# Kernel optimization log

Hardware: AMD Instinct MI355X
Metric: run time of the kernel (lower is better)

The kernel has to match this reference:

```python
import jax, jax.numpy as jnp
import numpy as np

N_IN, N_OUT, KNN, N_EL = 100000, 25000, 9, 200000
B, C_IN, C_OUT = 4, 8, 16


def setup_inputs() -> dict:
    key = jax.random.key(0)
    ks = jax.random.split(key, 16)
    M = N_OUT * KNN
    inp = {
        "features": jax.random.normal(ks[0], (B, C_IN, N_IN), jnp.float32),
        "domain_points": jax.random.uniform(ks[1], (N_IN, 2), jnp.float32),
        "range_points": jax.random.uniform(ks[2], (N_OUT, 2), jnp.float32),
        # kNN structure: each range point i has exactly KNN support edges
        "eval_idx_dst": jnp.repeat(jnp.arange(N_OUT, dtype=jnp.int32), KNN),
        "eval_idx_src": jax.random.randint(ks[3], (M,), 0, N_IN, jnp.int32),
        "element_list": jax.random.randint(ks[4], (N_EL, 3), 0, N_IN, jnp.int32),
        # Siren filter MLP: 2 -> 16 x5 -> C_IN*C_OUT (outermost linear)
        "siren_w_in": jax.random.normal(ks[5], (2, 16), jnp.float32) / jnp.sqrt(2.0),
        "siren_b_in": jax.random.normal(ks[6], (16,), jnp.float32) * 0.1,
        "siren_wh": jax.random.normal(ks[7], (4, 16, 16), jnp.float32) / 4.0,
        "siren_bh": jax.random.normal(ks[8], (4, 16), jnp.float32) * 0.1,
        "siren_w_out": jax.random.normal(ks[9], (16, C_IN * C_OUT), jnp.float32) / 4.0,
        "siren_b_out": jax.random.normal(ks[10], (C_IN * C_OUT,), jnp.float32) * 0.1,
        # weight_map: 6 -> 8 -> 8 -> 8 -> 3, all sigmoid
        "wm_w0": jax.random.normal(ks[11], (6, 8), jnp.float32) / jnp.sqrt(6.0),
        "wm_b0": jnp.zeros((8,), jnp.float32),
        "wm_w1": jax.random.normal(ks[12], (8, 8), jnp.float32) / jnp.sqrt(8.0),
        "wm_b1": jnp.zeros((8,), jnp.float32),
        "wm_w2": jax.random.normal(ks[13], (8, 8), jnp.float32) / jnp.sqrt(8.0),
        "wm_b2": jnp.zeros((8,), jnp.float32),
        "wm_w3": jax.random.normal(ks[14], (8, 3), jnp.float32) / jnp.sqrt(8.0),
        "wm_b3": jnp.zeros((3,), jnp.float32),
    }
    return inp


def reference(features, domain_points, range_points, eval_idx_src, eval_idx_dst,
              element_list, siren_w_in, siren_b_in, siren_wh, siren_bh,
              siren_w_out, siren_b_out, wm_w0, wm_b0, wm_w1, wm_b1,
              wm_w2, wm_b2, wm_w3, wm_b3):
    omega_0 = 1.0
    n_in = domain_points.shape[0]
    n_out = range_points.shape[0]
    c_in = features.shape[1]
    c_out = siren_w_out.shape[1] // c_in

    # --- eval_weight_map: per-element MLP + scatter_add to per-node weights ---
    el_pts = domain_points[element_list].reshape(element_list.shape[0], -1)  # [E, 6]
    h = jax.nn.sigmoid(el_pts @ wm_w0 + wm_b0)
    h = jax.nn.sigmoid(h @ wm_w1 + wm_b1)
    h = jax.nn.sigmoid(h @ wm_w2 + wm_b2)
    el_w = jax.nn.sigmoid(h @ wm_w3 + wm_b3)  # [E, 3]
    node_w = jax.ops.segment_sum(el_w.reshape(-1), element_list.reshape(-1),
                                 num_segments=n_in)  # [N_in]
    w = node_w[eval_idx_src]  # [M]

    # --- per-edge Siren filter on relative locations ---
    locs = range_points[eval_idx_dst] - domain_points[eval_idx_src]  # [M, 2]
    h = jnp.sin(omega_0 * (locs @ siren_w_in + siren_b_in))
    for i in range(siren_wh.shape[0]):  # fixed small layer count
        h = jnp.sin(omega_0 * (h @ siren_wh[i] + siren_bh[i]))
    filt = ((h @ siren_w_out + siren_b_out)
            .reshape(-1, c_in, c_out)) / c_in  # [M, C_in, C_out]

    # --- weighted gather -> contract -> scatter (quadrature integral) ---
    gathered = features[:, :, eval_idx_src]  # [B, C_in, M]
    values = jnp.einsum('n,nij,bin->bjn', w, filt, gathered)  # [B, C_out, M]
    seg = jax.ops.segment_sum(values.transpose(2, 0, 1), eval_idx_dst,
                              num_segments=n_out)  # [N_out, B, C_out]
    return seg.transpose(1, 2, 0)  # [B, C_out, N_out]
```

## Files before the change

kernel.cpp:

```cpp
#include <hip/hip_runtime.h>

#define N_IN   100000
#define N_OUT  25000
#define KNN    9
#define N_EL   200000
#define BB     4
#define C_IN   8
#define C_OUT  16

#define DPB  14
#define EPB  (DPB * KNN)
#define SOP  65
#define HST  17

__global__ void __launch_bounds__(256) elem_kernel(
    const int*   __restrict__ el,
    const float* __restrict__ dp,
    const float* __restrict__ w0, const float* __restrict__ b0,
    const float* __restrict__ w1, const float* __restrict__ b1,
    const float* __restrict__ w2, const float* __restrict__ b2,
    const float* __restrict__ w3, const float* __restrict__ b3,
    float* __restrict__ node_w)
{
    int e = blockIdx.x * 256 + threadIdx.x;
    if (e >= N_EL) return;
    int i0 = el[e*3+0], i1 = el[e*3+1], i2 = el[e*3+2];
    float2 p0 = ((const float2*)dp)[i0];
    float2 p1 = ((const float2*)dp)[i1];
    float2 p2 = ((const float2*)dp)[i2];
    float p[6] = { p0.x, p0.y, p1.x, p1.y, p2.x, p2.y };

    float h[8], h2[8];
#pragma unroll
    for (int k = 0; k < 8; ++k) {
        float t = b0[k];
#pragma unroll
        for (int j = 0; j < 6; ++j) t = fmaf(p[j], w0[j*8+k], t);
        h[k] = 1.f / (1.f + __expf(-t));
    }
#pragma unroll
    for (int k = 0; k < 8; ++k) {
        float t = b1[k];
#pragma unroll
        for (int j = 0; j < 8; ++j) t = fmaf(h[j], w1[j*8+k], t);
        h2[k] = 1.f / (1.f + __expf(-t));
    }
#pragma unroll
    for (int k = 0; k < 8; ++k) {
        float t = b2[k];
#pragma unroll
        for (int j = 0; j < 8; ++j) t = fmaf(h2[j], w2[j*8+k], t);
        h[k] = 1.f / (1.f + __expf(-t));
    }
    float o[3];
#pragma unroll
    for (int k = 0; k < 3; ++k) {
        float t = b3[k];
#pragma unroll
        for (int j = 0; j < 8; ++j) t = fmaf(h[j], w3[j*3+k], t);
        o[k] = 1.f / (1.f + __expf(-t));
    }
    atomicAdd(&node_w[i0], o[0]);
    atomicAdd(&node_w[i1], o[1]);
    atomicAdd(&node_w[i2], o[2]);
}

__global__ void __launch_bounds__(256) prep_kernel(
    const float* __restrict__ f, float* __restrict__ ft,
    const float* __restrict__ w_out, float* __restrict__ w_out_t,
    float* __restrict__ node_w)
{
    int n = blockIdx.x * 256 + threadIdx.x;
    if (n < C_IN * C_OUT * 16)
        w_out_t[n] = w_out[(n & 15) * 128 + (n >> 4)];
    if (n >= N_IN) return;
    node_w[n] = 0.f;
    float v[32];
#pragma unroll
    for (int c = 0; c < 32; ++c) v[c] = f[c * N_IN + n];
    float4* dst = (float4*)(ft + (size_t)n * 32);
#pragma unroll
    for (int q = 0; q < 8; ++q)
        dst[q] = make_float4(v[q], v[8+q], v[16+q], v[24+q]);
}

template <int FT>
__global__ void __launch_bounds__(256, 6) edge_kernel(
    const float* __restrict__ feat,
    const float* __restrict__ dp,
    const float* __restrict__ rp,
    const int*   __restrict__ src_idx,
    const float* __restrict__ node_w,
    const float* __restrict__ w_in,
    const float* __restrict__ b_in,
    const float* __restrict__ wh,
    const float* __restrict__ bh,
    const float* __restrict__ w_out,
    const float* __restrict__ w_out_t,
    const float* __restrict__ b_out,
    float* __restrict__ out)
{
    __shared__ float s_out[DPB * SOP];
    __shared__ float h_lds[EPB * HST];
    __shared__ int   s_src[EPB];
    __shared__ float s_scale[EPB];
    const int tid = threadIdx.x;

    for (int i = tid; i < DPB * SOP; i += 256) s_out[i] = 0.f;

    if (tid < EPB) {
        const int eg   = blockIdx.x * EPB + tid;
        const int ldst = tid / KNN;
        const int dst  = blockIdx.x * DPB + ldst;
        const bool valid = (dst < N_OUT);
        const int ce   = valid ? eg : 0;
        const int src  = src_idx[ce];
        s_src[tid]   = src;
        const float wn = node_w[src];
        s_scale[tid] = valid ? wn * 0.125f : 0.f;

        const float2 rpt = ((const float2*)rp)[valid ? dst : 0];
        const float2 dpt = ((const float2*)dp)[src];
        const float lx = rpt.x - dpt.x;
        const float ly = rpt.y - dpt.y;

        float h[16];
#pragma unroll
        for (int k = 0; k < 16; ++k)
            h[k] = __sinf(fmaf(lx, w_in[k], fmaf(ly, w_in[16+k], b_in[k])));

#pragma unroll
        for (int L = 0; L < 4; ++L) {
            float h2[16];
#pragma unroll
            for (int k = 0; k < 16; ++k) {
                float t = bh[L*16 + k];
#pragma unroll
                for (int j = 0; j < 16; ++j)
                    t = fmaf(h[j], wh[L*256 + j*16 + k], t);
                h2[k] = t;
            }
#pragma unroll
            for (int k = 0; k < 16; ++k) h[k] = __sinf(h2[k]);
        }
#pragma unroll
        for (int k = 0; k < 16; ++k) h_lds[tid * HST + k] = h[k];
    }
    __syncthreads();

#pragma unroll 1
    for (int r = 0; r < 2; ++r) {
        const int item = tid + r * 256;
        const int e    = item & 127;
        const int jq   = __builtin_amdgcn_readfirstlane(item >> 7);
        if (e < EPB) {
            const int   src   = s_src[e];
            const float scale = s_scale[e];
            float hh[16];
#pragma unroll
            for (int k = 0; k < 16; ++k) hh[k] = h_lds[e * HST + k];

            const float4* fp4 = (const float4*)(feat + (size_t)src * 32);
            float acc[16];
#pragma unroll
            for (int t = 0; t < 16; ++t) acc[t] = 0.f;
#pragma unroll
            for (int i = 0; i < C_IN; ++i) {
                float4 gb;
                if (FT) {
                    gb = fp4[i];
                } else {
                    gb = make_float4(feat[(0*8+i) * N_IN + src],
                                     feat[(1*8+i) * N_IN + src],
                                     feat[(2*8+i) * N_IN + src],
                                     feat[(3*8+i) * N_IN + src]);
                }
#pragma unroll
                for (int jj = 0; jj < 4; ++jj) {
                    const int col = i*16 + jq*4 + jj;
                    float f = b_out[col];
#pragma unroll
                    for (int k = 0; k < 16; ++k)
                        f = fmaf(hh[k],
                                 FT ? w_out_t[col*16 + k] : w_out[k*128 + col],
                                 f);
                    f *= scale;
                    acc[0*4+jj] = fmaf(f, gb.x, acc[0*4+jj]);
                    acc[1*4+jj] = fmaf(f, gb.y, acc[1*4+jj]);
                    acc[2*4+jj] = fmaf(f, gb.z, acc[2*4+jj]);
                    acc[3*4+jj] = fmaf(f, gb.w, acc[3*4+jj]);
                }
            }
            const int ldst = e / KNN;
#pragma unroll
            for (int b = 0; b < BB; ++b)
#pragma unroll
                for (int jj = 0; jj < 4; ++jj)
                    atomicAdd(&s_out[ldst * SOP + b*16 + jq*4 + jj],
                              acc[b*4+jj]);
        }
    }
    __syncthreads();

    const int dst0 = blockIdx.x * DPB;
#pragma unroll 1
    for (int i = tid; i < DPB * 64; i += 256) {
        const int d = i % DPB;
        const int c = i / DPB;
        const int gdst = dst0 + d;
        if (gdst < N_OUT)
            out[(size_t)c * N_OUT + gdst] = s_out[d * SOP + c];
    }
}

extern "C" void kernel_launch(void* const* d_in, const int* in_sizes, int n_in,
                              void* d_out, int out_size, void* d_ws, size_t ws_size,
                              hipStream_t stream)
{
    (void)in_sizes; (void)n_in; (void)out_size;
    const float* features = (const float*)d_in[0];
    const float* dp       = (const float*)d_in[1];
    const float* rp       = (const float*)d_in[2];
    const int*   src_idx  = (const int*)d_in[4];
    const int*   el       = (const int*)d_in[5];
    const float* w_in     = (const float*)d_in[6];
    const float* b_in     = (const float*)d_in[7];
    const float* wh       = (const float*)d_in[8];
    const float* bh       = (const float*)d_in[9];
    const float* w_out    = (const float*)d_in[10];
    const float* b_out    = (const float*)d_in[11];
    const float* wm_w0    = (const float*)d_in[12];
    const float* wm_b0    = (const float*)d_in[13];
    const float* wm_w1    = (const float*)d_in[14];
    const float* wm_b1    = (const float*)d_in[15];
    const float* wm_w2    = (const float*)d_in[16];
    const float* wm_b2    = (const float*)d_in[17];
    const float* wm_w3    = (const float*)d_in[18];
    const float* wm_b3    = (const float*)d_in[19];
    float* out = (float*)d_out;

    size_t off0 = 0;
    size_t off1 = (off0 + (size_t)N_IN * sizeof(float) + 511) & ~(size_t)511;
    size_t off2 = (off1 + (size_t)N_IN * 32 * sizeof(float) + 511) & ~(size_t)511;
    size_t need = off2 + (size_t)2048 * sizeof(float);
    float* node_w  = (float*)((char*)d_ws + off0);
    float* feat_t  = (float*)((char*)d_ws + off1);
    float* w_out_t = (float*)((char*)d_ws + off2);
    const bool use_t = (ws_size >= need);

    const int edge_blocks = (N_OUT + DPB - 1) / DPB;

    if (use_t) {
        prep_kernel<<<(N_IN + 255) / 256, 256, 0, stream>>>(
            features, feat_t, w_out, w_out_t, node_w);
        elem_kernel<<<(N_EL + 255) / 256, 256, 0, stream>>>(
            el, dp, wm_w0, wm_b0, wm_w1, wm_b1, wm_w2, wm_b2, wm_w3, wm_b3, node_w);
        edge_kernel<1><<<edge_blocks, 256, 0, stream>>>(
            feat_t, dp, rp, src_idx, node_w,
            w_in, b_in, wh, bh, w_out, w_out_t, b_out, out);
    } else {
        hipMemsetAsync(node_w, 0, (size_t)N_IN * sizeof(float), stream);
        elem_kernel<<<(N_EL + 255) / 256, 256, 0, stream>>>(
            el, dp, wm_w0, wm_b0, wm_w1, wm_b1, wm_w2, wm_b2, wm_w3, wm_b3, node_w);
        edge_kernel<0><<<edge_blocks, 256, 0, stream>>>(
            features, dp, rp, src_idx, node_w,
            w_in, b_in, wh, bh, w_out, (const float*)nullptr, b_out, out);
    }
}
```

Baseline: 260.4 us.

## Split fused edge kernel into full-parallel Siren kernel and einsum kernel

The per-edge Siren MLP, which previously ran on only 126 of 256 threads per block, moves into its own kernel with one thread per edge. Its hidden activations go to a channel-major workspace buffer. A separate einsum kernel then reads them back coalesced and does the contraction with all threads busy. This targets the idle lanes during the sin-heavy MLP phase. In exchange it adds a launch and a workspace round-trip of about 14 MB, and the path is only taken when the workspace is large enough.

```diff
diff --git a/kernel.cpp b/kernel.cpp
--- a/kernel.cpp
+++ b/kernel.cpp
@@ -7,10 +7,14 @@
 #define BB     4
 #define C_IN   8
 #define C_OUT  16
-
-#define DPB  14
-#define EPB  (DPB * KNN)
+#define M_EDGE (N_OUT * KNN)
+#define MP     225024
+
 #define SOP  65
+#define DPB2 7
+#define EPB2 (DPB2 * KNN)
+#define DPBF 14
+#define EPBF (DPBF * KNN)
 #define HST  17
 
 __global__ void __launch_bounds__(256) elem_kernel(
@@ -84,51 +88,142 @@
         dst[q] = make_float4(v[q], v[8+q], v[16+q], v[24+q]);
 }
 
-template <int FT>
-__global__ void __launch_bounds__(256, 6) edge_kernel(
-    const float* __restrict__ feat,
+__global__ void __launch_bounds__(256) siren_kernel(
     const float* __restrict__ dp,
     const float* __restrict__ rp,
     const int*   __restrict__ src_idx,
-    const float* __restrict__ node_w,
     const float* __restrict__ w_in,
     const float* __restrict__ b_in,
     const float* __restrict__ wh,
     const float* __restrict__ bh,
-    const float* __restrict__ w_out,
+    float* __restrict__ h_t)
+{
+    int e = blockIdx.x * 256 + threadIdx.x;
+    if (e >= M_EDGE) return;
+    const int dst = e / KNN;
+    const int src = src_idx[e];
+    const float2 rpt = ((const float2*)rp)[dst];
+    const float2 dpt = ((const float2*)dp)[src];
+    const float lx = rpt.x - dpt.x;
+    const float ly = rpt.y - dpt.y;
+
+    float h[16];
+#pragma unroll
+    for (int k = 0; k < 16; ++k)
+        h[k] = __sinf(fmaf(lx, w_in[k], fmaf(ly, w_in[16+k], b_in[k])));
+#pragma unroll
+    for (int L = 0; L < 4; ++L) {
+        float h2[16];
+#pragma unroll
+        for (int k = 0; k < 16; ++k) {
+            float t = bh[L*16 + k];
+#pragma unroll
+            for (int j = 0; j < 16; ++j)
+                t = fmaf(h[j], wh[L*256 + j*16 + k], t);
+            h2[k] = t;
+        }
+#pragma unroll
+        for (int k = 0; k < 16; ++k) h[k] = __sinf(h2[k]);
+    }
+#pragma unroll
+    for (int k = 0; k < 16; ++k) h_t[k * MP + e] = h[k];
+}
+
+__global__ void __launch_bounds__(256) einsum_kernel(
+    const float* __restrict__ feat_t,
+    const int*   __restrict__ src_idx,
+    const float* __restrict__ node_w,
+    const float* __restrict__ h_t,
     const float* __restrict__ w_out_t,
     const float* __restrict__ b_out,
     float* __restrict__ out)
 {
-    __shared__ float s_out[DPB * SOP];
-    __shared__ float h_lds[EPB * HST];
-    __shared__ int   s_src[EPB];
-    __shared__ float s_scale[EPB];
+    __shared__ float s_out[DPB2 * SOP];
+    const int tid  = threadIdx.x;
+    const int lane = tid & 63;
+    const int jq   = tid >> 6;
+
+    for (int i = tid; i < DPB2 * SOP; i += 256) s_out[i] = 0.f;
+    __syncthreads();
+
+    const int  dst0  = blockIdx.x * DPB2;
+    const int  e_loc = (lane < EPB2) ? lane : 0;
+    const int  dst   = dst0 + e_loc / KNN;
+    const bool valid = (lane < EPB2) && (dst < N_OUT);
+    const int  ce    = valid ? (blockIdx.x * EPB2 + e_loc) : 0;
+    const int  src   = src_idx[ce];
+    const float scale = valid ? node_w[src] * 0.125f : 0.f;
+
+    float hh[16];
+#pragma unroll
+    for (int k = 0; k < 16; ++k) hh[k] = h_t[k * MP + ce];
+
+    const float4* fp4 = (const float4*)(feat_t + (size_t)src * 32);
+    float acc[16];
+#pragma unroll
+    for (int t = 0; t < 16; ++t) acc[t] = 0.f;
+#pragma unroll
+    for (int i = 0; i < C_IN; ++i) {
+        const float4 gb = fp4[i];
+#pragma unroll
+        for (int jj = 0; jj < 4; ++jj) {
+            const int col = i*16 + jq*4 + jj;
+            float f = b_out[col];
+#pragma unroll
+            for (int k = 0; k < 16; ++k)
+                f = fmaf(hh[k], w_out_t[col*16 + k], f);
+            f *= scale;
+            acc[0*4+jj] = fmaf(f, gb.x, acc[0*4+jj]);
+            acc[1*4+jj] = fmaf(f, gb.y, acc[1*4+jj]);
+            acc[2*4+jj] = fmaf(f, gb.z, acc[2*4+jj]);
+            acc[3*4+jj] = fmaf(f, gb.w, acc[3*4+jj]);
+        }
+    }
+    const int ldst = e_loc / KNN;
+#pragma unroll
+    for (int b = 0; b < BB; ++b)
+#pragma unroll
+        for (int jj = 0; jj < 4; ++jj)
+            atomicAdd(&s_out[ldst * SOP + b*16 + jq*4 + jj], acc[b*4+jj]);
+    __syncthreads();
+
+    for (int i = tid; i < DPB2 * 64; i += 256) {
+        const int d = i % DPB2;
+        const int c = i / DPB2;
+        const int g = dst0 + d;
+        if (g < N_OUT) out[(size_t)c * N_OUT + g] = s_out[d * SOP + c];
+    }
+}
+
+__global__ void __launch_bounds__(256, 6) edge_fused_kernel(
+    const float* __restrict__ feat, const float* __restrict__ dp,
+    const float* __restrict__ rp, const int* __restrict__ src_idx,
+    const float* __restrict__ node_w, const float* __restrict__ w_in,
+    const float* __restrict__ b_in, const float* __restrict__ wh,
+    const float* __restrict__ bh, const float* __restrict__ w_out,
+    const float* __restrict__ b_out, float* __restrict__ out)
+{
+    __shared__ float s_out[DPBF * SOP];
+    __shared__ float h_lds[EPBF * HST];
+    __shared__ int   s_src[EPBF];
+    __shared__ float s_scale[EPBF];
     const int tid = threadIdx.x;
-
-    for (int i = tid; i < DPB * SOP; i += 256) s_out[i] = 0.f;
-
-    if (tid < EPB) {
-        const int eg   = blockIdx.x * EPB + tid;
-        const int ldst = tid / KNN;
-        const int dst  = blockIdx.x * DPB + ldst;
+    for (int i = tid; i < DPBF * SOP; i += 256) s_out[i] = 0.f;
+    if (tid < EPBF) {
+        const int eg = blockIdx.x * EPBF + tid;
+        const int dst = blockIdx.x * DPBF + tid / KNN;
         const bool valid = (dst < N_OUT);
-        const int ce   = valid ? eg : 0;
-        const int src  = src_idx[ce];
-        s_src[tid]   = src;
-        const float wn = node_w[src];
-        s_scale[tid] = valid ? wn * 0.125f : 0.f;
-
+        const int ce = valid ? eg : 0;
+        const int src = src_idx[ce];
+        s_src[tid] = src;
+        s_scale[tid] = valid ? node_w[src] * 0.125f : 0.f;
         const float2 rpt = ((const float2*)rp)[valid ? dst : 0];
         const float2 dpt = ((const float2*)dp)[src];
-        const float lx = rpt.x - dpt.x;
-        const float ly = rpt.y - dpt.y;
-
+        const float lx = rpt.x - dpt.x, ly = rpt.y - dpt.y;
         float h[16];
 #pragma unroll
         for (int k = 0; k < 16; ++k)
             h[k] = __sinf(fmaf(lx, w_in[k], fmaf(ly, w_in[16+k], b_in[k])));
-
 #pragma unroll
         for (int L = 0; L < 4; ++L) {
             float h2[16];
@@ -136,8 +231,7 @@
             for (int k = 0; k < 16; ++k) {
                 float t = bh[L*16 + k];
 #pragma unroll
-                for (int j = 0; j < 16; ++j)
-                    t = fmaf(h[j], wh[L*256 + j*16 + k], t);
+                for (int j = 0; j < 16; ++j) t = fmaf(h[j], wh[L*256 + j*16 + k], t);
                 h2[k] = t;
             }
 #pragma unroll
@@ -147,43 +241,30 @@
         for (int k = 0; k < 16; ++k) h_lds[tid * HST + k] = h[k];
     }
     __syncthreads();
-
 #pragma unroll 1
     for (int r = 0; r < 2; ++r) {
         const int item = tid + r * 256;
-        const int e    = item & 127;
-        const int jq   = __builtin_amdgcn_readfirstlane(item >> 7);
-        if (e < EPB) {
-            const int   src   = s_src[e];
+        const int e = item & 127;
+        const int jq = __builtin_amdgcn_readfirstlane(item >> 7);
+        if (e < EPBF) {
+            const int src = s_src[e];
             const float scale = s_scale[e];
             float hh[16];
 #pragma unroll
             for (int k = 0; k < 16; ++k) hh[k] = h_lds[e * HST + k];
-
-            const float4* fp4 = (const float4*)(feat + (size_t)src * 32);
             float acc[16];
 #pragma unroll
             for (int t = 0; t < 16; ++t) acc[t] = 0.f;
 #pragma unroll
             for (int i = 0; i < C_IN; ++i) {
-                float4 gb;
-                if (FT) {
-                    gb = fp4[i];
-                } else {
-                    gb = make_float4(feat[(0*8+i) * N_IN + src],
-                                     feat[(1*8+i) * N_IN + src],
-                                     feat[(2*8+i) * N_IN + src],
-                                     feat[(3*8+i) * N_IN + src]);
-                }
+                float4 gb = make_float4(feat[(0*8+i)*N_IN+src], feat[(1*8+i)*N_IN+src],
+                                        feat[(2*8+i)*N_IN+src], feat[(3*8+i)*N_IN+src]);
 #pragma unroll
                 for (int jj = 0; jj < 4; ++jj) {
                     const int col = i*16 + jq*4 + jj;
                     float f = b_out[col];
 #pragma unroll
-                    for (int k = 0; k < 16; ++k)
-                        f = fmaf(hh[k],
-                                 FT ? w_out_t[col*16 + k] : w_out[k*128 + col],
-                                 f);
+                    for (int k = 0; k < 16; ++k) f = fmaf(hh[k], w_out[k*128 + col], f);
                     f *= scale;
                     acc[0*4+jj] = fmaf(f, gb.x, acc[0*4+jj]);
                     acc[1*4+jj] = fmaf(f, gb.y, acc[1*4+jj]);
@@ -196,20 +277,16 @@
             for (int b = 0; b < BB; ++b)
 #pragma unroll
                 for (int jj = 0; jj < 4; ++jj)
-                    atomicAdd(&s_out[ldst * SOP + b*16 + jq*4 + jj],
-                              acc[b*4+jj]);
+                    atomicAdd(&s_out[ldst * SOP + b*16 + jq*4 + jj], acc[b*4+jj]);
         }
     }
     __syncthreads();
-
-    const int dst0 = blockIdx.x * DPB;
+    const int dst0 = blockIdx.x * DPBF;
 #pragma unroll 1
-    for (int i = tid; i < DPB * 64; i += 256) {
-        const int d = i % DPB;
-        const int c = i / DPB;
-        const int gdst = dst0 + d;
-        if (gdst < N_OUT)
-            out[(size_t)c * N_OUT + gdst] = s_out[d * SOP + c];
+    for (int i = tid; i < DPBF * 64; i += 256) {
+        const int d = i % DPBF, c = i / DPBF;
+        const int g = dst0 + d;
+        if (g < N_OUT) out[(size_t)c * N_OUT + g] = s_out[d * SOP + c];
     }
 }
 
@@ -242,28 +319,29 @@
     size_t off0 = 0;
     size_t off1 = (off0 + (size_t)N_IN * sizeof(float) + 511) & ~(size_t)511;
     size_t off2 = (off1 + (size_t)N_IN * 32 * sizeof(float) + 511) & ~(size_t)511;
-    size_t need = off2 + (size_t)2048 * sizeof(float);
+    size_t off3 = (off2 + (size_t)2048 * sizeof(float) + 511) & ~(size_t)511;
+    size_t need = off3 + (size_t)16 * MP * sizeof(float);
     float* node_w  = (float*)((char*)d_ws + off0);
     float* feat_t  = (float*)((char*)d_ws + off1);
     float* w_out_t = (float*)((char*)d_ws + off2);
+    float* h_t     = (float*)((char*)d_ws + off3);
     const bool use_t = (ws_size >= need);
-
-    const int edge_blocks = (N_OUT + DPB - 1) / DPB;
 
     if (use_t) {
         prep_kernel<<<(N_IN + 255) / 256, 256, 0, stream>>>(
             features, feat_t, w_out, w_out_t, node_w);
         elem_kernel<<<(N_EL + 255) / 256, 256, 0, stream>>>(
             el, dp, wm_w0, wm_b0, wm_w1, wm_b1, wm_w2, wm_b2, wm_w3, wm_b3, node_w);
-        edge_kernel<1><<<edge_blocks, 256, 0, stream>>>(
-            feat_t, dp, rp, src_idx, node_w,
-            w_in, b_in, wh, bh, w_out, w_out_t, b_out, out);
+        siren_kernel<<<(M_EDGE + 255) / 256, 256, 0, stream>>>(
+            dp, rp, src_idx, w_in, b_in, wh, bh, h_t);
+        einsum_kernel<<<(N_OUT + DPB2 - 1) / DPB2, 256, 0, stream>>>(
+            feat_t, src_idx, node_w, h_t, w_out_t, b_out, out);
     } else {
         hipMemsetAsync(node_w, 0, (size_t)N_IN * sizeof(float), stream);
         elem_kernel<<<(N_EL + 255) / 256, 256, 0, stream>>>(
             el, dp, wm_w0, wm_b0, wm_w1, wm_b1, wm_w2, wm_b2, wm_w3, wm_b3, node_w);
-        edge_kernel<0><<<edge_blocks, 256, 0, stream>>>(
+        edge_fused_kernel<<<(N_OUT + DPBF - 1) / DPBF, 256, 0, stream>>>(
             features, dp, rp, src_idx, node_w,
-            w_in, b_in, wh, bh, w_out, (const float*)nullptr, b_out, out);
-    }
-}
+            w_in, b_in, wh, bh, w_out, b_out, out);
+    }
+}
```

Result: slower. 303.7 us (+16.6%).
